# Performance work log

Hardware: AMD Instinct MI355X
Metric: run time of the kernel (lower is better)

Reference implementation:

```python
import jax, jax.numpy as jnp
import numpy as np

IN_DIM, OUT_DIM = 4096, 11008
NUM_SUBDIM, KS = 1376, 256
DS = OUT_DIM // NUM_SUBDIM  # 8
BATCH = 32


def setup_inputs() -> dict:
    key = jax.random.key(0)
    k1, k2, k3, k4 = jax.random.split(key, 4)
    x = jax.random.normal(k1, (BATCH, IN_DIM), dtype=jnp.float32)
    vectors = jax.random.normal(k2, (NUM_SUBDIM, KS, DS), dtype=jnp.float32)
    bias = jax.random.normal(k3, (OUT_DIM,), dtype=jnp.float32)
    indexes = jax.random.randint(k4, (IN_DIM, NUM_SUBDIM), 0, KS, dtype=jnp.int64)
    return {"x": x, "vectors": vectors, "bias": bias, "indexes": indexes}


def reference(x, vectors, bias, indexes):
    in_dim, num_subdim = indexes.shape
    ds = vectors.shape[-1]
    # PQ dequant: gather codewords per (row, subspace) -> [in_dim, num_subdim, Ds]
    # vectors[d, indexes[i, d]] via broadcast of arange(num_subdim) against indexes.
    dims = jnp.arange(num_subdim)
    weight = vectors[dims, indexes].reshape(in_dim, num_subdim * ds)  # [in_dim, out_dim]
    return x @ weight + bias
```

## Files before the change

### kernel.cpp

```cpp
#include <hip/hip_runtime.h>

#define IN_DIM  4096
#define OUT_DIM 11008
#define NSUB    1376
#define KSQ     256
#define DSUB    8
#define BATCH   32

#define DTILE   8
#define NTILE   64
#define KC      64
#define KSPLIT  16
#define KPB     (IN_DIM / KSPLIT)
#define NCHUNK  (KPB / KC)
#define NBLK    (OUT_DIM / NTILE)

typedef unsigned short ushort_t;
typedef unsigned int   uint_t;
typedef unsigned char  uchar_t;
typedef __attribute__((ext_vector_type(8))) short bf16x8;
typedef __attribute__((ext_vector_type(4))) float f32x4;

#define VEC_N    (NSUB * KSQ * DSUB)
#define XBF_OFF  (VEC_N * 2)
#define IDXT_OFF (XBF_OFF + BATCH * IN_DIM * 2)
#define SLAB_OFF (IDXT_OFF + NSUB * IN_DIM)
#define PREP_V   (VEC_N / 2)
#define PREP_X   (BATCH * IN_DIM / 2)
#define PREP_N   (PREP_V + PREP_X)

__device__ __forceinline__ ushort_t f2bf(float f) {
    union { float f; uint_t u; } a; a.f = f;
    uint_t u = a.u;
    u += 0x7fffu + ((u >> 16) & 1u);
    return (ushort_t)(u >> 16);
}

__global__ __launch_bounds__(256) void pq_prep(
    const float* __restrict__ x, const float* __restrict__ vecs,
    uint_t* __restrict__ vbf, uint_t* __restrict__ xbf)
{
    int tid = blockIdx.x * 256 + threadIdx.x;
    if (tid < PREP_V) {
        float2 v = ((const float2*)vecs)[tid];
        vbf[tid] = (uint_t)f2bf(v.x) | ((uint_t)f2bf(v.y) << 16);
    } else {
        int i = tid - PREP_V;
        float2 v = ((const float2*)x)[i];
        xbf[i] = (uint_t)f2bf(v.x) | ((uint_t)f2bf(v.y) << 16);
    }
}

__global__ __launch_bounds__(256) void pq_idxT(
    const int* __restrict__ idx, uchar_t* __restrict__ idx8T)
{
    __shared__ uchar_t sT[32][144];
    const int k0 = blockIdx.x * 128, d0 = blockIdx.y * 32, t = threadIdx.x;
    #pragma unroll
    for (int p = 0; p < 16; ++p) {
        int f = p * 256 + t;
        int kk = f >> 5, dd = f & 31;
        sT[dd][kk] = (uchar_t)idx[(size_t)(k0 + kk) * NSUB + d0 + dd];
    }
    __syncthreads();
    int dd = t >> 3, seg = t & 7;
    uint4 v = *(const uint4*)&sT[dd][seg * 16];
    *(uint4*)&idx8T[(size_t)(d0 + dd) * IN_DIM + k0 + seg * 16] = v;
}

__global__ __launch_bounds__(256, 4) void pq_main(
    const ushort_t* __restrict__ xbf, const uint4* __restrict__ vbf4,
    const uchar_t* __restrict__ idx8T, float* __restrict__ slab)
{
    __shared__ uint4  sV4[4 * 512];
    __shared__ uint_t sW32[4 * 16 * 32];

    const int t    = threadIdx.x;
    const int w    = t >> 6;
    const int lane = t & 63;
    const int nblk = blockIdx.x;
    const int kblk = blockIdx.y;
    const int d0   = nblk * DTILE;
    const int kbase = kblk * KPB;

    const int l15 = lane & 15;
    const int l4  = lane >> 4;
    const int dl  = lane >> 5;
    const int q   = lane & 31;

    {
        const size_t src0 = (size_t)(d0 + w * 2) * KSQ;
        #pragma unroll
        for (int p = 0; p < 8; ++p)
            sV4[w * 512 + p * 64 + lane] = vbf4[src0 + p * 64 + lane];
    }

    bf16x8 A[2][8];
    #pragma unroll
    for (int mt = 0; mt < 2; ++mt)
        #pragma unroll
        for (int kk = 0; kk < 8; ++kk)
            A[mt][kk] = *(const bf16x8*)
                &xbf[(size_t)(mt * 16 + l15) * IN_DIM + kbase + kk * 32 + l4 * 8];

    f32x4 acc[2];
    acc[0] = (f32x4)0.0f; acc[1] = (f32x4)0.0f;

    const uchar_t* idxrow = idx8T + (size_t)(d0 + w * 2 + dl) * IN_DIM + kbase;
    const int vbase = w * 512 + dl * 256;
    const int Rbase = (w * 16 + dl * 8) * 32;

    #pragma unroll
    for (int c = 0; c < NCHUNK; ++c) {
        uint_t bb = *(const ushort_t*)&idxrow[c * KC + q * 2];
        uint4 g0 = sV4[vbase + (bb & 255)];
        uint4 g1 = sV4[vbase + (bb >> 8)];

        #pragma unroll
        for (int j = 0; j < 8; ++j) {
            const uint_t sel = (j & 1) ? 0x07060302u : 0x05040100u;
            uint_t a0 = (j >> 1) == 0 ? g0.x : (j >> 1) == 1 ? g0.y : (j >> 1) == 2 ? g0.z : g0.w;
            uint_t a1 = (j >> 1) == 0 ? g1.x : (j >> 1) == 1 ? g1.y : (j >> 1) == 2 ? g1.z : g1.w;
            uint_t wv = __builtin_amdgcn_perm(a1, a0, sel);
            int dw = ((((q >> 2) ^ j) << 2) | (q & 3));
            sW32[Rbase + j * 32 + dw] = wv;
        }

        #pragma unroll
        for (int kq = 0; kq < 2; ++kq) {
            int u16 = (kq * 4 + l4) ^ (l15 & 7);
            bf16x8 B = *(const bf16x8*)
                ((const char*)sW32 + (w * 16 + l15) * 128 + u16 * 16);
            #pragma unroll
            for (int mt = 0; mt < 2; ++mt)
                acc[mt] = __builtin_amdgcn_mfma_f32_16x16x32_bf16(
                    A[mt][c * 2 + kq], B, acc[mt], 0, 0, 0);
        }
    }

    float* sl = slab + (size_t)kblk * BATCH * OUT_DIM;
    const int col = nblk * NTILE + w * 16 + l15;
    #pragma unroll
    for (int mt = 0; mt < 2; ++mt)
        #pragma unroll
        for (int r = 0; r < 4; ++r)
            sl[(size_t)(mt * 16 + l4 * 4 + r) * OUT_DIM + col] = acc[mt][r];
}

__global__ __launch_bounds__(256) void pq_reduce(
    const float* __restrict__ slab, const float* __restrict__ bias,
    float* __restrict__ out)
{
    int i = blockIdx.x * 256 + threadIdx.x;
    int m = i / (OUT_DIM / 4), n4 = i % (OUT_DIM / 4);
    float4 s = ((const float4*)bias)[n4];
    #pragma unroll
    for (int kb = 0; kb < KSPLIT; ++kb) {
        float4 v = ((const float4*)slab)[(size_t)(kb * BATCH + m) * (OUT_DIM / 4) + n4];
        s.x += v.x; s.y += v.y; s.z += v.z; s.w += v.w;
    }
    ((float4*)out)[(size_t)m * (OUT_DIM / 4) + n4] = s;
}

extern "C" void kernel_launch(void* const* d_in, const int* in_sizes, int n_in,
                              void* d_out, int out_size, void* d_ws, size_t ws_size,
                              hipStream_t stream) {
    const float* x    = (const float*)d_in[0];
    const float* vecs = (const float*)d_in[1];
    const float* bias = (const float*)d_in[2];
    const int*   idx  = (const int*)d_in[3];
    float* out = (float*)d_out;

    uint_t*  vbf   = (uint_t*)d_ws;
    uint_t*  xbf   = (uint_t*)((char*)d_ws + XBF_OFF);
    uchar_t* idx8T = (uchar_t*)((char*)d_ws + IDXT_OFF);
    float*   slab  = (float*)((char*)d_ws + SLAB_OFF);

    pq_prep<<<PREP_N / 256, 256, 0, stream>>>(x, vecs, vbf, xbf);
    pq_idxT<<<dim3(IN_DIM / 128, NSUB / 32), 256, 0, stream>>>(idx, idx8T);
    pq_main<<<dim3(NBLK, KSPLIT), 256, 0, stream>>>(
        (const ushort_t*)xbf, (const uint4*)vbf, idx8T, slab);
    pq_reduce<<<(BATCH * OUT_DIM / 4) / 256, 256, 0, stream>>>(slab, bias, out);
}
```

Baseline: 116.1 us.

## Merge prep kernels, remap main grid per XCD, prefetch indices into registers

Merges the bf16 conversion and index-transpose kernels into a single launch to remove one kernel launch and its gap. Remaps the main GEMM grid to a 1D id so that all k-split blocks of one n-tile land on the same XCD, improving L2 reuse of codebooks and indices. Hoists the codebook and index global loads ahead of the LDS stores so the loads are issued together and overlap. It pads the grid to 176 n-blocks, so some blocks exit early, and holds more live registers.

```diff
diff --git a/kernel.cpp b/kernel.cpp
--- a/kernel.cpp
+++ b/kernel.cpp
@@ -14,6 +14,8 @@
 #define KPB     (IN_DIM / KSPLIT)
 #define NCHUNK  (KPB / KC)
 #define NBLK    (OUT_DIM / NTILE)
+#define NBLKP   176
+#define GRID_MAIN (NBLKP * KSPLIT)
 
 typedef unsigned short ushort_t;
 typedef unsigned int   uint_t;
@@ -28,6 +30,8 @@
 #define PREP_V   (VEC_N / 2)
 #define PREP_X   (BATCH * IN_DIM / 2)
 #define PREP_N   (PREP_V + PREP_X)
+#define PACK_BLK (PREP_N / 256)
+#define IDXT_BLK ((IN_DIM / 128) * (NSUB / 32))
 
 __device__ __forceinline__ ushort_t f2bf(float f) {
     union { float f; uint_t u; } a; a.f = f;
@@ -38,24 +42,28 @@
 
 __global__ __launch_bounds__(256) void pq_prep(
     const float* __restrict__ x, const float* __restrict__ vecs,
-    uint_t* __restrict__ vbf, uint_t* __restrict__ xbf)
-{
-    int tid = blockIdx.x * 256 + threadIdx.x;
-    if (tid < PREP_V) {
-        float2 v = ((const float2*)vecs)[tid];
-        vbf[tid] = (uint_t)f2bf(v.x) | ((uint_t)f2bf(v.y) << 16);
-    } else {
-        int i = tid - PREP_V;
-        float2 v = ((const float2*)x)[i];
-        xbf[i] = (uint_t)f2bf(v.x) | ((uint_t)f2bf(v.y) << 16);
-    }
-}
-
-__global__ __launch_bounds__(256) void pq_idxT(
-    const int* __restrict__ idx, uchar_t* __restrict__ idx8T)
+    const int* __restrict__ idx,
+    uint_t* __restrict__ vbf, uint_t* __restrict__ xbf,
+    uchar_t* __restrict__ idx8T)
 {
     __shared__ uchar_t sT[32][144];
-    const int k0 = blockIdx.x * 128, d0 = blockIdx.y * 32, t = threadIdx.x;
+    const int t = threadIdx.x;
+
+    if (blockIdx.x < PACK_BLK) {
+        int tid = blockIdx.x * 256 + t;
+        if (tid < PREP_V) {
+            float2 v = ((const float2*)vecs)[tid];
+            vbf[tid] = (uint_t)f2bf(v.x) | ((uint_t)f2bf(v.y) << 16);
+        } else {
+            int i = tid - PREP_V;
+            float2 v = ((const float2*)x)[i];
+            xbf[i] = (uint_t)f2bf(v.x) | ((uint_t)f2bf(v.y) << 16);
+        }
+        return;
+    }
+
+    const int bid = blockIdx.x - PACK_BLK;
+    const int k0 = (bid & 31) * 128, d0 = (bid >> 5) * 32;
     #pragma unroll
     for (int p = 0; p < 16; ++p) {
         int f = p * 256 + t;
@@ -75,11 +83,16 @@
     __shared__ uint4  sV4[4 * 512];
     __shared__ uint_t sW32[4 * 16 * 32];
 
+    const int id   = blockIdx.x;
+    const int xcd  = id & 7;
+    const int slot = id >> 3;
+    const int kblk = slot & 15;
+    const int nblk = (slot >> 4) * 8 + xcd;
+    if (nblk >= NBLK) return;
+
     const int t    = threadIdx.x;
     const int w    = t >> 6;
     const int lane = t & 63;
-    const int nblk = blockIdx.x;
-    const int kblk = blockIdx.y;
     const int d0   = nblk * DTILE;
     const int kbase = kblk * KPB;
 
@@ -88,12 +101,11 @@
     const int dl  = lane >> 5;
     const int q   = lane & 31;
 
-    {
-        const size_t src0 = (size_t)(d0 + w * 2) * KSQ;
-        #pragma unroll
-        for (int p = 0; p < 8; ++p)
-            sV4[w * 512 + p * 64 + lane] = vbf4[src0 + p * 64 + lane];
-    }
+    uint4 vst[8];
+    const size_t src0 = (size_t)(d0 + w * 2) * KSQ;
+    #pragma unroll
+    for (int p = 0; p < 8; ++p)
+        vst[p] = vbf4[src0 + p * 64 + lane];
 
     bf16x8 A[2][8];
     #pragma unroll
@@ -103,18 +115,28 @@
             A[mt][kk] = *(const bf16x8*)
                 &xbf[(size_t)(mt * 16 + l15) * IN_DIM + kbase + kk * 32 + l4 * 8];
 
+    const uchar_t* idxrow = idx8T + (size_t)(d0 + w * 2 + dl) * IN_DIM + kbase;
+    uint_t bb[NCHUNK];
+    #pragma unroll
+    for (int c = 0; c < NCHUNK; ++c)
+        bb[c] = *(const ushort_t*)&idxrow[c * KC + q * 2];
+
+    #pragma unroll
+    for (int p = 0; p < 8; ++p)
+        sV4[w * 512 + p * 64 + lane] = vst[p];
+
+    __builtin_amdgcn_sched_barrier(0);
+
     f32x4 acc[2];
     acc[0] = (f32x4)0.0f; acc[1] = (f32x4)0.0f;
 
-    const uchar_t* idxrow = idx8T + (size_t)(d0 + w * 2 + dl) * IN_DIM + kbase;
     const int vbase = w * 512 + dl * 256;
     const int Rbase = (w * 16 + dl * 8) * 32;
 
     #pragma unroll
     for (int c = 0; c < NCHUNK; ++c) {
-        uint_t bb = *(const ushort_t*)&idxrow[c * KC + q * 2];
-        uint4 g0 = sV4[vbase + (bb & 255)];
-        uint4 g1 = sV4[vbase + (bb >> 8)];
+        uint4 g0 = sV4[vbase + (bb[c] & 255)];
+        uint4 g1 = sV4[vbase + (bb[c] >> 8)];
 
         #pragma unroll
         for (int j = 0; j < 8; ++j) {
@@ -176,9 +198,8 @@
     uchar_t* idx8T = (uchar_t*)((char*)d_ws + IDXT_OFF);
     float*   slab  = (float*)((char*)d_ws + SLAB_OFF);
 
-    pq_prep<<<PREP_N / 256, 256, 0, stream>>>(x, vecs, vbf, xbf);
-    pq_idxT<<<dim3(IN_DIM / 128, NSUB / 32), 256, 0, stream>>>(idx, idx8T);
-    pq_main<<<dim3(NBLK, KSPLIT), 256, 0, stream>>>(
+    pq_prep<<<PACK_BLK + IDXT_BLK, 256, 0, stream>>>(x, vecs, idx, vbf, xbf, idx8T);
+    pq_main<<<GRID_MAIN, 256, 0, stream>>>(
         (const ushort_t*)xbf, (const uint4*)vbf, idx8T, slab);
     pq_reduce<<<(BATCH * OUT_DIM / 4) / 256, 256, 0, stream>>>(slab, bias, out);
 }
```

New measurement: 116.6 us. Within noise of the previous version (+0.5%).

## Fuse prep, GEMM and reduce into one cooperative persistent kernel

Applied to the files above, without the earlier changes.

Replaces the four separate launches with a single cooperative kernel that runs persistent blocks through prep (bf16 conversion plus index transpose), the PQ-gather MFMA phase, and the split-K reduction, separated by grid syncs. Blocks take contiguous tile ranges so the codebook slice in shared memory is reloaded only when the output block changes, and index bytes are prefetched into registers. The aim is to cut launch gaps and codebook reloads. The cost is two grid-wide barriers and fewer resident blocks for latency hiding.

```diff
diff --git a/kernel.cpp b/kernel.cpp
--- a/kernel.cpp
+++ b/kernel.cpp
@@ -1,4 +1,7 @@
 #include <hip/hip_runtime.h>
+#include <hip/hip_cooperative_groups.h>
+
+namespace cg = cooperative_groups;
 
 #define IN_DIM  4096
 #define OUT_DIM 11008
@@ -14,6 +17,7 @@
 #define KPB     (IN_DIM / KSPLIT)
 #define NCHUNK  (KPB / KC)
 #define NBLK    (OUT_DIM / NTILE)
+#define NTILES  (NBLK * KSPLIT)
 
 typedef unsigned short ushort_t;
 typedef unsigned int   uint_t;
@@ -25,9 +29,9 @@
 #define XBF_OFF  (VEC_N * 2)
 #define IDXT_OFF (XBF_OFF + BATCH * IN_DIM * 2)
 #define SLAB_OFF (IDXT_OFF + NSUB * IN_DIM)
-#define PREP_V   (VEC_N / 2)
-#define PREP_X   (BATCH * IN_DIM / 2)
-#define PREP_N   (PREP_V + PREP_X)
+
+#define SMEM_BYTES 40960
+#define IDXT_TILES ((IN_DIM / 128) * (NSUB / 32))
 
 __device__ __forceinline__ ushort_t f2bf(float f) {
     union { float f; uint_t u; } a; a.f = f;
@@ -36,130 +40,194 @@
     return (ushort_t)(u >> 16);
 }
 
-__global__ __launch_bounds__(256) void pq_prep(
+__device__ __forceinline__ void phase_prep(
     const float* __restrict__ x, const float* __restrict__ vecs,
-    uint_t* __restrict__ vbf, uint_t* __restrict__ xbf)
-{
-    int tid = blockIdx.x * 256 + threadIdx.x;
-    if (tid < PREP_V) {
-        float2 v = ((const float2*)vecs)[tid];
-        vbf[tid] = (uint_t)f2bf(v.x) | ((uint_t)f2bf(v.y) << 16);
-    } else {
-        int i = tid - PREP_V;
-        float2 v = ((const float2*)x)[i];
-        xbf[i] = (uint_t)f2bf(v.x) | ((uint_t)f2bf(v.y) << 16);
-    }
-}
-
-__global__ __launch_bounds__(256) void pq_idxT(
-    const int* __restrict__ idx, uchar_t* __restrict__ idx8T)
-{
-    __shared__ uchar_t sT[32][144];
-    const int k0 = blockIdx.x * 128, d0 = blockIdx.y * 32, t = threadIdx.x;
-    #pragma unroll
-    for (int p = 0; p < 16; ++p) {
-        int f = p * 256 + t;
-        int kk = f >> 5, dd = f & 31;
-        sT[dd][kk] = (uchar_t)idx[(size_t)(k0 + kk) * NSUB + d0 + dd];
-    }
-    __syncthreads();
-    int dd = t >> 3, seg = t & 7;
-    uint4 v = *(const uint4*)&sT[dd][seg * 16];
-    *(uint4*)&idx8T[(size_t)(d0 + dd) * IN_DIM + k0 + seg * 16] = v;
-}
-
-__global__ __launch_bounds__(256, 4) void pq_main(
-    const ushort_t* __restrict__ xbf, const uint4* __restrict__ vbf4,
+    const int* __restrict__ idx,
+    uint_t* __restrict__ vbf, uint_t* __restrict__ xbf,
+    uchar_t* __restrict__ idx8T, char* smem, int t, int bid, int G)
+{
+    const int g = bid * 256 + t, stride = G * 256;
+
+    for (int i = g; i < VEC_N / 4; i += stride) {
+        float4 v = ((const float4*)vecs)[i];
+        uint2 o;
+        o.x = (uint_t)f2bf(v.x) | ((uint_t)f2bf(v.y) << 16);
+        o.y = (uint_t)f2bf(v.z) | ((uint_t)f2bf(v.w) << 16);
+        ((uint2*)vbf)[i] = o;
+    }
+    for (int i = g; i < BATCH * IN_DIM / 4; i += stride) {
+        float4 v = ((const float4*)x)[i];
+        uint2 o;
+        o.x = (uint_t)f2bf(v.x) | ((uint_t)f2bf(v.y) << 16);
+        o.y = (uint_t)f2bf(v.z) | ((uint_t)f2bf(v.w) << 16);
+        ((uint2*)xbf)[i] = o;
+    }
+
+    uchar_t (*sT)[144] = (uchar_t (*)[144])smem;
+    for (int tile = bid; tile < IDXT_TILES; tile += G) {
+        const int k0 = (tile & 31) * 128, d0 = (tile >> 5) * 32;
+        __syncthreads();
+        #pragma unroll
+        for (int p = 0; p < 16; ++p) {
+            int f = p * 256 + t, kk = f >> 5, dd = f & 31;
+            sT[dd][kk] = (uchar_t)idx[(size_t)(k0 + kk) * NSUB + d0 + dd];
+        }
+        __syncthreads();
+        int dd = t >> 3, seg = t & 7;
+        uint4 v = *(const uint4*)&sT[dd][seg * 16];
+        *(uint4*)&idx8T[(size_t)(d0 + dd) * IN_DIM + k0 + seg * 16] = v;
+    }
+}
+
+__device__ __forceinline__ void phase_main(
+    const ushort_t* __restrict__ xbfu, const uint4* __restrict__ vbf4,
+    const uchar_t* __restrict__ idx8T, float* __restrict__ slab,
+    char* smem, int t, int bid, int G)
+{
+    uint4*  sV4  = (uint4*)smem;
+    uint_t* sW32 = (uint_t*)(smem + 32768);
+
+    const int w = t >> 6, lane = t & 63;
+    const int l15 = lane & 15, l4 = lane >> 4, dl = lane >> 5, q = lane & 31;
+
+    const int tt0 = (int)(((long)bid * NTILES) / G);
+    const int tt1 = (int)(((long)(bid + 1) * NTILES) / G);
+    int cur_nblk = -1;
+
+    for (int tile = tt0; tile < tt1; ++tile) {
+        const int nblk = tile >> 4, kblk = tile & 15;
+        const int d0 = nblk * DTILE, kbase = kblk * KPB;
+
+        if (nblk != cur_nblk) {
+            cur_nblk = nblk;
+            const size_t src0 = (size_t)(d0 + w * 2) * KSQ;
+            #pragma unroll
+            for (int h = 0; h < 2; ++h) {
+                uint4 vst[4];
+                #pragma unroll
+                for (int p = 0; p < 4; ++p)
+                    vst[p] = vbf4[src0 + (h * 4 + p) * 64 + lane];
+                #pragma unroll
+                for (int p = 0; p < 4; ++p)
+                    sV4[w * 512 + (h * 4 + p) * 64 + lane] = vst[p];
+            }
+        }
+
+        bf16x8 A[2][8];
+        #pragma unroll
+        for (int mt = 0; mt < 2; ++mt)
+            #pragma unroll
+            for (int kk = 0; kk < 8; ++kk)
+                A[mt][kk] = *(const bf16x8*)
+                    &xbfu[(size_t)(mt * 16 + l15) * IN_DIM + kbase + kk * 32 + l4 * 8];
+
+        const uchar_t* idxrow = idx8T + (size_t)(d0 + w * 2 + dl) * IN_DIM + kbase;
+        uint_t bb[NCHUNK];
+        #pragma unroll
+        for (int c = 0; c < NCHUNK; ++c)
+            bb[c] = *(const ushort_t*)&idxrow[c * KC + q * 2];
+
+        f32x4 acc[2];
+        acc[0] = (f32x4)0.0f; acc[1] = (f32x4)0.0f;
+        const int vbase = w * 512 + dl * 256;
+        const int Rbase = (w * 16 + dl * 8) * 32;
+
+        #pragma unroll
+        for (int c = 0; c < NCHUNK; ++c) {
+            uint4 g0 = sV4[vbase + (bb[c] & 255)];
+            uint4 g1 = sV4[vbase + (bb[c] >> 8)];
+
+            #pragma unroll
+            for (int j = 0; j < 8; ++j) {
+                const uint_t sel = (j & 1) ? 0x07060302u : 0x05040100u;
+                uint_t a0 = (j >> 1) == 0 ? g0.x : (j >> 1) == 1 ? g0.y : (j >> 1) == 2 ? g0.z : g0.w;
+                uint_t a1 = (j >> 1) == 0 ? g1.x : (j >> 1) == 1 ? g1.y : (j >> 1) == 2 ? g1.z : g1.w;
+                uint_t wv = __builtin_amdgcn_perm(a1, a0, sel);
+                int dw = ((((q >> 2) ^ j) << 2) | (q & 3));
+                sW32[Rbase + j * 32 + dw] = wv;
+            }
+
+            #pragma unroll
+            for (int kq = 0; kq < 2; ++kq) {
+                int u16 = (kq * 4 + l4) ^ (l15 & 7);
+                bf16x8 B = *(const bf16x8*)
+                    ((const char*)sW32 + (w * 16 + l15) * 128 + u16 * 16);
+                #pragma unroll
+                for (int mt = 0; mt < 2; ++mt)
+                    acc[mt] = __builtin_amdgcn_mfma_f32_16x16x32_bf16(
+                        A[mt][c * 2 + kq], B, acc[mt], 0, 0, 0);
+            }
+        }
+
+        float* sl = slab + (size_t)kblk * BATCH * OUT_DIM;
+        const int col = nblk * NTILE + w * 16 + l15;
+        #pragma unroll
+        for (int mt = 0; mt < 2; ++mt)
+            #pragma unroll
+            for (int r = 0; r < 4; ++r)
+                sl[(size_t)(mt * 16 + l4 * 4 + r) * OUT_DIM + col] = acc[mt][r];
+    }
+}
+
+__device__ __forceinline__ void phase_reduce(
+    const float* __restrict__ slab, const float* __restrict__ bias,
+    float* __restrict__ out, int g, int stride)
+{
+    for (int i = g; i < BATCH * OUT_DIM / 4; i += stride) {
+        int m = i / (OUT_DIM / 4), n4 = i - m * (OUT_DIM / 4);
+        float4 s = ((const float4*)bias)[n4];
+        #pragma unroll
+        for (int kb = 0; kb < KSPLIT; ++kb) {
+            float4 v = ((const float4*)slab)[(size_t)(kb * BATCH + m) * (OUT_DIM / 4) + n4];
+            s.x += v.x; s.y += v.y; s.z += v.z; s.w += v.w;
+        }
+        ((float4*)out)[i] = s;
+    }
+}
+
+__global__ __launch_bounds__(256) void pq_all(
+    const float* __restrict__ x, const float* __restrict__ vecs,
+    const float* __restrict__ bias, const int* __restrict__ idx,
+    uint_t* __restrict__ vbf, uint_t* __restrict__ xbf,
+    uchar_t* __restrict__ idx8T, float* __restrict__ slab,
+    float* __restrict__ out)
+{
+    extern __shared__ __align__(16) char smem[];
+    const int t = threadIdx.x, bid = blockIdx.x, G = gridDim.x;
+
+    phase_prep(x, vecs, idx, vbf, xbf, idx8T, smem, t, bid, G);
+    __threadfence();
+    cg::this_grid().sync();
+
+    phase_main((const ushort_t*)xbf, (const uint4*)vbf, idx8T, slab, smem, t, bid, G);
+    __threadfence();
+    cg::this_grid().sync();
+
+    phase_reduce(slab, bias, out, bid * 256 + t, G * 256);
+}
+
+__global__ __launch_bounds__(256) void pq_p1(
+    const float* __restrict__ x, const float* __restrict__ vecs,
+    const int* __restrict__ idx, uint_t* __restrict__ vbf,
+    uint_t* __restrict__ xbf, uchar_t* __restrict__ idx8T)
+{
+    extern __shared__ __align__(16) char smem[];
+    phase_prep(x, vecs, idx, vbf, xbf, idx8T, smem, threadIdx.x, blockIdx.x, gridDim.x);
+}
+
+__global__ __launch_bounds__(256) void pq_p2(
+    const ushort_t* __restrict__ xbfu, const uint4* __restrict__ vbf4,
     const uchar_t* __restrict__ idx8T, float* __restrict__ slab)
 {
-    __shared__ uint4  sV4[4 * 512];
-    __shared__ uint_t sW32[4 * 16 * 32];
-
-    const int t    = threadIdx.x;
-    const int w    = t >> 6;
-    const int lane = t & 63;
-    const int nblk = blockIdx.x;
-    const int kblk = blockIdx.y;
-    const int d0   = nblk * DTILE;
-    const int kbase = kblk * KPB;
-
-    const int l15 = lane & 15;
-    const int l4  = lane >> 4;
-    const int dl  = lane >> 5;
-    const int q   = lane & 31;
-
-    {
-        const size_t src0 = (size_t)(d0 + w * 2) * KSQ;
-        #pragma unroll
-        for (int p = 0; p < 8; ++p)
-            sV4[w * 512 + p * 64 + lane] = vbf4[src0 + p * 64 + lane];
-    }
-
-    bf16x8 A[2][8];
-    #pragma unroll
-    for (int mt = 0; mt < 2; ++mt)
-        #pragma unroll
-        for (int kk = 0; kk < 8; ++kk)
-            A[mt][kk] = *(const bf16x8*)
-                &xbf[(size_t)(mt * 16 + l15) * IN_DIM + kbase + kk * 32 + l4 * 8];
-
-    f32x4 acc[2];
-    acc[0] = (f32x4)0.0f; acc[1] = (f32x4)0.0f;
-
-    const uchar_t* idxrow = idx8T + (size_t)(d0 + w * 2 + dl) * IN_DIM + kbase;
-    const int vbase = w * 512 + dl * 256;
-    const int Rbase = (w * 16 + dl * 8) * 32;
-
-    #pragma unroll
-    for (int c = 0; c < NCHUNK; ++c) {
-        uint_t bb = *(const ushort_t*)&idxrow[c * KC + q * 2];
-        uint4 g0 = sV4[vbase + (bb & 255)];
-        uint4 g1 = sV4[vbase + (bb >> 8)];
-
-        #pragma unroll
-        for (int j = 0; j < 8; ++j) {
-            const uint_t sel = (j & 1) ? 0x07060302u : 0x05040100u;
-            uint_t a0 = (j >> 1) == 0 ? g0.x : (j >> 1) == 1 ? g0.y : (j >> 1) == 2 ? g0.z : g0.w;
-            uint_t a1 = (j >> 1) == 0 ? g1.x : (j >> 1) == 1 ? g1.y : (j >> 1) == 2 ? g1.z : g1.w;
-            uint_t wv = __builtin_amdgcn_perm(a1, a0, sel);
-            int dw = ((((q >> 2) ^ j) << 2) | (q & 3));
-            sW32[Rbase + j * 32 + dw] = wv;
-        }
-
-        #pragma unroll
-        for (int kq = 0; kq < 2; ++kq) {
-            int u16 = (kq * 4 + l4) ^ (l15 & 7);
-            bf16x8 B = *(const bf16x8*)
-                ((const char*)sW32 + (w * 16 + l15) * 128 + u16 * 16);
-            #pragma unroll
-            for (int mt = 0; mt < 2; ++mt)
-                acc[mt] = __builtin_amdgcn_mfma_f32_16x16x32_bf16(
-                    A[mt][c * 2 + kq], B, acc[mt], 0, 0, 0);
-        }
-    }
-
-    float* sl = slab + (size_t)kblk * BATCH * OUT_DIM;
-    const int col = nblk * NTILE + w * 16 + l15;
-    #pragma unroll
-    for (int mt = 0; mt < 2; ++mt)
-        #pragma unroll
-        for (int r = 0; r < 4; ++r)
-            sl[(size_t)(mt * 16 + l4 * 4 + r) * OUT_DIM + col] = acc[mt][r];
-}
-
-__global__ __launch_bounds__(256) void pq_reduce(
+    extern __shared__ __align__(16) char smem[];
+    phase_main(xbfu, vbf4, idx8T, slab, smem, threadIdx.x, blockIdx.x, gridDim.x);
+}
+
+__global__ __launch_bounds__(256) void pq_p3(
     const float* __restrict__ slab, const float* __restrict__ bias,
     float* __restrict__ out)
 {
-    int i = blockIdx.x * 256 + threadIdx.x;
-    int m = i / (OUT_DIM / 4), n4 = i % (OUT_DIM / 4);
-    float4 s = ((const float4*)bias)[n4];
-    #pragma unroll
-    for (int kb = 0; kb < KSPLIT; ++kb) {
-        float4 v = ((const float4*)slab)[(size_t)(kb * BATCH + m) * (OUT_DIM / 4) + n4];
-        s.x += v.x; s.y += v.y; s.z += v.z; s.w += v.w;
-    }
-    ((float4*)out)[(size_t)m * (OUT_DIM / 4) + n4] = s;
+    phase_reduce(slab, bias, out, blockIdx.x * 256 + threadIdx.x, gridDim.x * 256);
 }
 
 extern "C" void kernel_launch(void* const* d_in, const int* in_sizes, int n_in,
@@ -176,9 +244,27 @@
     uchar_t* idx8T = (uchar_t*)((char*)d_ws + IDXT_OFF);
     float*   slab  = (float*)((char*)d_ws + SLAB_OFF);
 
-    pq_prep<<<PREP_N / 256, 256, 0, stream>>>(x, vecs, vbf, xbf);
-    pq_idxT<<<dim3(IN_DIM / 128, NSUB / 32), 256, 0, stream>>>(idx, idx8T);
-    pq_main<<<dim3(NBLK, KSPLIT), 256, 0, stream>>>(
-        (const ushort_t*)xbf, (const uint4*)vbf, idx8T, slab);
-    pq_reduce<<<(BATCH * OUT_DIM / 4) / 256, 256, 0, stream>>>(slab, bias, out);
-}
+    static int G = 0;
+    if (G == 0) {
+        int bpc = 0;
+        if (hipOccupancyMaxActiveBlocksPerMultiprocessor(
+                &bpc, pq_all, 256, (size_t)SMEM_BYTES) != hipSuccess || bpc < 1)
+            bpc = 2;
+        if (bpc > 4) bpc = 4;
+        G = bpc * 256;
+    }
+
+    void* args[] = {(void*)&x, (void*)&vecs, (void*)&bias, (void*)&idx,
+                    (void*)&vbf, (void*)&xbf, (void*)&idx8T, (void*)&slab,
+                    (void*)&out};
+    hipError_t e = hipLaunchCooperativeKernel(
+        reinterpret_cast<const void*>(pq_all), dim3(G), dim3(256),
+        args, (unsigned)SMEM_BYTES, stream);
+
+    if (e != hipSuccess) {
+        pq_p1<<<2048, 256, SMEM_BYTES, stream>>>(x, vecs, idx, vbf, xbf, idx8T);
+        pq_p2<<<1024, 256, SMEM_BYTES, stream>>>(
+            (const ushort_t*)xbf, (const uint4*)vbf, idx8T, slab);
+        pq_p3<<<(BATCH * OUT_DIM / 4 + 255) / 256, 256, 0, stream>>>(slab, bias, out);
+    }
+}
```

After: 351.5 us. 203% more time.
